# Kernel tuning notes

Hardware: AMD Instinct MI355X
Metric: run time of the kernel (lower is better)

## Reference

```python
import jax, jax.numpy as jnp
import numpy as np

B, H, W, DM = 4, 64, 64, 96
DS, DC, K = 16, 3, 4
DI = DM            # expand = 1.0
DTR = 6            # ceil(96/16)


def setup_inputs() -> dict:
    key = jax.random.key(0)
    ks = jax.random.split(key, 12)
    s = 0.02
    # dt bias init exactly as MS2D.dt_init: dt ~ exp(U*(log(max)-log(min))+log(min)); inv softplus
    dt = jnp.exp(jax.random.uniform(ks[5], (K, DI)) * (np.log(0.1) - np.log(0.001)) + np.log(0.001))
    dt = jnp.clip(dt, 1e-4, None)
    inv_dt = dt + jnp.log(-jnp.expm1(-dt))
    A_logs = jnp.log(jnp.broadcast_to(jnp.arange(1, DS + 1, dtype=jnp.float32), (K, DI, DS)))
    return {
        "x": jax.random.normal(ks[0], (B, H, W, DM), jnp.float32),
        "in_proj_w": jax.random.normal(ks[1], (2 * DI, DM), jnp.float32) * s,
        "conv_w": jax.random.normal(ks[2], (DI, 1, DC, DC), jnp.float32) * s,
        "conv_b": jnp.zeros((DI,), jnp.float32),
        "x_proj_weight": jax.random.normal(ks[3], (K, DTR + 2 * DS, DI), jnp.float32) * s,
        "dt_projs_weight": jax.random.uniform(ks[4], (K, DI, DTR), minval=-1.0, maxval=1.0) * (DTR ** -0.5),
        "dt_projs_bias": inv_dt,
        "A_logs": A_logs,
        "Ds": jnp.ones((K, DI), jnp.float32),
        "out_norm_w": jnp.ones((DI,), jnp.float32),
        "out_norm_b": jnp.zeros((DI,), jnp.float32),
        "out_proj_w": jax.random.normal(ks[6], (DM, DI), jnp.float32) * s,
    }


def _ms2d(x, in_proj_w, conv_w, conv_b, x_proj_weight, dt_projs_weight,
          dt_projs_bias, A_logs, Ds, out_norm_w, out_norm_b, out_proj_w):
    Bb, Hh, Ww, _ = x.shape
    L = Hh * Ww
    # in_proj -> (x, z) gating split
    xz = x @ in_proj_w.T                      # (B,H,W,2*DI)
    xc, z = jnp.split(xz, 2, axis=-1)
    xc = jnp.transpose(xc, (0, 3, 1, 2))      # (B,DI,H,W)
    xc = jax.lax.conv_general_dilated(
        xc, conv_w, (1, 1), 'SAME', feature_group_count=xc.shape[1],
        dimension_numbers=('NCHW', 'OIHW', 'NCHW')) + conv_b[None, :, None, None]
    xc = jax.nn.silu(xc)
    d = xc.shape[1]
    # 4-directional scan sequences: hw, wh, and their reverses
    x_hw = xc.reshape(Bb, d, L)
    x_wh = jnp.transpose(xc, (0, 1, 3, 2)).reshape(Bb, d, L)
    x2 = jnp.stack([x_hw, x_wh], axis=1)          # (B,2,d,L)
    xs = jnp.concatenate([x2, jnp.flip(x2, axis=-1)], axis=1)  # (B,4,d,L)
    x_dbl = jnp.einsum('bkdl,kcd->bkcl', xs, x_proj_weight)
    dtr = dt_projs_weight.shape[2]
    n = A_logs.shape[2]
    dts, Bs, Cs = jnp.split(x_dbl, [dtr, dtr + n], axis=2)     # (B,4,r,L),(B,4,N,L),(B,4,N,L)
    dts = jnp.einsum('bkrl,kdr->bkdl', dts, dt_projs_weight)
    delta = jax.nn.softplus(dts + dt_projs_bias[None, :, :, None])  # (B,4,d,L)
    A = -jnp.exp(A_logs)                                        # (4,d,N)
    # time-major for scan
    u_t = jnp.moveaxis(xs, -1, 0)       # (L,B,4,d)
    dl_t = jnp.moveaxis(delta, -1, 0)
    B_t = jnp.moveaxis(Bs, -1, 0)       # (L,B,4,N)
    C_t = jnp.moveaxis(Cs, -1, 0)

    def step(h, inp):                   # h: (B,4,d,N)
        u, dl, b, c = inp
        dA = jnp.exp(dl[..., None] * A)
        h = h * dA + (dl * u)[..., None] * b[:, :, None, :]
        y = jnp.einsum('bkdn,bkn->bkd', h, c)
        return h, y

    h0 = jnp.zeros((Bb, 4, d, n), xs.dtype)
    _, ys = jax.lax.scan(step, h0, (u_t, dl_t, B_t, C_t))
    ys = jnp.moveaxis(ys, 0, -1)        # (B,4,d,L)
    ys = ys + Ds[None, :, :, None] * xs  # skip D*u
    inv_y = jnp.flip(ys[:, 2:4], axis=-1)

    def wh2hw(t):  # undo the (W,H) raster order
        return jnp.transpose(t.reshape(Bb, d, Ww, Hh), (0, 1, 3, 2)).reshape(Bb, d, L)

    y = ys[:, 0] + inv_y[:, 0] + wh2hw(ys[:, 1]) + wh2hw(inv_y[:, 1])
    y = jnp.transpose(y, (0, 2, 1)).reshape(Bb, Hh, Ww, d)
    mu = y.mean(-1, keepdims=True)
    var = y.var(-1, keepdims=True)
    y = (y - mu) / jnp.sqrt(var + 1e-5) * out_norm_w + out_norm_b
    y = y * jax.nn.silu(z)
    return y @ out_proj_w.T


def reference(x, in_proj_w, conv_w, conv_b, x_proj_weight, dt_projs_weight,
              dt_projs_bias, A_logs, Ds, out_norm_w, out_norm_b, out_proj_w):
    return _ms2d(x, in_proj_w, conv_w, conv_b, x_proj_weight, dt_projs_weight,
                 dt_projs_bias, A_logs, Ds, out_norm_w, out_norm_b, out_proj_w)
```

## Files before the change

### kernel.cpp

```cpp
#include <hip/hip_runtime.h>
#include <math.h>


#define LQ 4096
#define NCH 128
#define LCH 32

__device__ __forceinline__ float sigmoid_f(float x){ return 1.0f/(1.0f + __expf(-x)); }
__device__ __forceinline__ float silu_f(float x){ return x * sigmoid_f(x); }
__device__ __forceinline__ float softplus_f(float x){ return (x > 20.0f) ? x : __logf(1.0f + __expf(x)); }

__device__ __forceinline__ int pos_of(int k, int i){
  switch(k & 3){
    case 0: return i;
    case 1: return ((i & 63) << 6) | (i >> 6);
    case 2: return LQ - 1 - i;
    default: { int j = LQ - 1 - i; return ((j & 63) << 6) | (j >> 6); }
  }
}

__device__ __forceinline__ void pow8(float r, int nh, float* e){
  e[0]=r;
  e[1]=r*r;
  e[2]=e[1]*r;
  e[3]=e[1]*e[1];
  e[4]=e[3]*r;
  e[5]=e[3]*e[1];
  e[6]=e[3]*e[2];
  e[7]=e[3]*e[3];
  float m = nh ? e[7] : 1.0f;
  #pragma unroll
  for (int j=0;j<8;j++) e[j] *= m;
}

__global__ __launch_bounds__(256) void k_inproj(const float* __restrict__ x,
                                                const float* __restrict__ wproj,
                                                float* __restrict__ xc,
                                                float* __restrict__ zb){
  __shared__ float a_s[64*97];
  __shared__ float w_s[96*97];
  const int t = threadIdx.x;
  const int row0 = (blockIdx.x >> 1) * 64;
  const int ch = blockIdx.x & 1;
  for (int e = t*4; e < 64*96; e += 1024){
    float4 v = *(const float4*)(x + (size_t)row0*96 + e);
    int r = e/96, c = e%96;
    float* p = a_s + r*97 + c;
    p[0]=v.x; p[1]=v.y; p[2]=v.z; p[3]=v.w;
  }
  for (int e = t*4; e < 96*96; e += 1024){
    float4 v = *(const float4*)(wproj + (size_t)ch*96*96 + e);
    int r = e/96, c = e%96;
    float* p = w_s + r*97 + c;
    p[0]=v.x; p[1]=v.y; p[2]=v.z; p[3]=v.w;
  }
  __syncthreads();
  const int tr = t >> 5, tc = t & 31;
  float acc[8][3];
  #pragma unroll
  for (int i=0;i<8;i++){
    #pragma unroll
    for (int j=0;j<3;j++) acc[i][j]=0.f;
  }
  for (int kk=0; kk<96; kk++){
    float a[8], b[3];
    #pragma unroll
    for (int i=0;i<8;i++) a[i] = a_s[(tr*8+i)*97+kk];
    #pragma unroll
    for (int j=0;j<3;j++) b[j] = w_s[(tc*3+j)*97+kk];
    #pragma unroll
    for (int i=0;i<8;i++){
      #pragma unroll
      for (int j=0;j<3;j++) acc[i][j] += a[i]*b[j];
    }
  }
  float* dst = ch ? zb : xc;
  #pragma unroll
  for (int i=0;i<8;i++){
    int row = row0 + tr*8 + i;
    #pragma unroll
    for (int j=0;j<3;j++) dst[(size_t)row*96 + tc*3 + j] = acc[i][j];
  }
}

__global__ __launch_bounds__(256) void k_conv(const float* __restrict__ xc,
                                              const float* __restrict__ cw,
                                              const float* __restrict__ cb,
                                              float* __restrict__ u){
  int e = blockIdx.x*256 + threadIdx.x;
  int d0 = (e % 24) * 4;
  int p = e / 24;
  int w = p & 63, h = (p >> 6) & 63, b = p >> 12;
  float cwv[4][9];
  #pragma unroll
  for (int q=0;q<4;q++){
    #pragma unroll
    for (int tp=0;tp<9;tp++) cwv[q][tp] = cw[(d0+q)*9+tp];
  }
  float4 acc = make_float4(cb[d0], cb[d0+1], cb[d0+2], cb[d0+3]);
  #pragma unroll
  for (int kh=0; kh<3; kh++){
    int hh = h + kh - 1;
    if (hh < 0 || hh > 63) continue;
    #pragma unroll
    for (int kw=0; kw<3; kw++){
      int ww = w + kw - 1;
      if (ww < 0 || ww > 63) continue;
      float4 v = *(const float4*)(xc + ((size_t)((b<<12) + (hh<<6) + ww))*96 + d0);
      int tp = kh*3+kw;
      acc.x += v.x*cwv[0][tp]; acc.y += v.y*cwv[1][tp];
      acc.z += v.z*cwv[2][tp]; acc.w += v.w*cwv[3][tp];
    }
  }
  float4 o = make_float4(silu_f(acc.x), silu_f(acc.y), silu_f(acc.z), silu_f(acc.w));
  *(float4*)(u + (size_t)p*96 + d0) = o;
}

__global__ __launch_bounds__(128) void k_proj(const float* __restrict__ u,
                                              const float* __restrict__ xpw,
                                              float* __restrict__ dts,
                                              float* __restrict__ Bsb,
                                              float* __restrict__ Csb){
  __shared__ float u_s[64*97];
  __shared__ float w_s[40*97];
  const int t = threadIdx.x;
  const int blk = blockIdx.x;
  const int pt = blk & 63, k = (blk >> 6) & 3, b = blk >> 8;
  const int p0 = pt * 64;
  for (int e = t*4; e < 64*96; e += 512){
    int pp = e/96, c = e%96;
    float4 v = *(const float4*)(u + ((size_t)((b<<12) + p0 + pp))*96 + c);
    float* p = u_s + pp*97 + c;
    p[0]=v.x; p[1]=v.y; p[2]=v.z; p[3]=v.w;
  }
  for (int e = t*4; e < 40*96; e += 512){
    int r = e/96, c = e%96;
    float4 v = (r < 38) ? *(const float4*)(xpw + (k*38+r)*96 + c)
                        : make_float4(0,0,0,0);
    float* p = w_s + r*97 + c;
    p[0]=v.x; p[1]=v.y; p[2]=v.z; p[3]=v.w;
  }
  __syncthreads();
  const int posg = t & 15, cg = t >> 4;
  float acc[4][5];
  #pragma unroll
  for (int i=0;i<4;i++){
    #pragma unroll
    for (int j=0;j<5;j++) acc[i][j]=0.f;
  }
  for (int dd=0; dd<96; dd++){
    float uu[4], wv[5];
    #pragma unroll
    for (int i=0;i<4;i++) uu[i] = u_s[(posg*4+i)*97+dd];
    #pragma unroll
    for (int j=0;j<5;j++) wv[j] = w_s[(cg*5+j)*97+dd];
    #pragma unroll
    for (int i=0;i<4;i++){
      #pragma unroll
      for (int j=0;j<5;j++) acc[i][j] += uu[i]*wv[j];
    }
  }
  #pragma unroll
  for (int i=0;i<4;i++){
    int p = p0 + posg*4 + i;
    int base = ((b*4+k)<<12) + p;
    #pragma unroll
    for (int j=0;j<5;j++){
      int c = cg*5 + j;
      float v = acc[i][j];
      if (c < 6)       dts[(size_t)base*6 + c] = v;
      else if (c < 22) Bsb[(size_t)base*16 + (c-6)] = v;
      else if (c < 38) Csb[(size_t)base*16 + (c-22)] = v;
    }
  }
}

__global__ __launch_bounds__(384) void k_scanA(const float* __restrict__ u,
                                               const float* __restrict__ dts,
                                               const float* __restrict__ Bsb,
                                               const float* __restrict__ dtw_g,
                                               const float* __restrict__ dtb_g,
                                               const float* __restrict__ Alogs,
                                               float* __restrict__ S,
                                               float* __restrict__ sumd){
  __shared__ float du_s[64*96];
  __shared__ float r_s[64*96];
  __shared__ float dt_s[64*8];
  __shared__ float B_s[64*16];
  __shared__ float sd_part[4*96];
  const int t = threadIdx.x;
  const int blk = blockIdx.x;
  const int bk = blk >> 6;
  const int k = bk & 3, b = bk >> 2;
  const int chunk0 = (blk & 63) << 1;
  for (int e = t*4; e < 64*96; e += 1536){
    int row = e/96, c = e%96;
    int p = pos_of(k, (chunk0 + (row>>5))*LCH + (row&31));
    float4 v = *(const float4*)(u + ((size_t)((b<<12)+p))*96 + c);
    float* dst = du_s + row*96 + c;
    dst[0]=v.x; dst[1]=v.y; dst[2]=v.z; dst[3]=v.w;
  }
  {
    int row = t/6, j = t - row*6;
    int p = pos_of(k, (chunk0 + (row>>5))*LCH + (row&31));
    dt_s[row*8+j] = dts[((size_t)((bk<<12)+p))*6 + j];
  }
  if (t < 256){
    int row = t>>2, q = t&3;
    int p = pos_of(k, (chunk0 + (row>>5))*LCH + (row&31));
    float4 v = *(const float4*)(Bsb + ((size_t)((bk<<12)+p))*16 + q*4);
    *(float4*)(B_s + row*16 + q*4) = v;
  }
  __syncthreads();
  {
    const int d = t % 96, g = t / 96;
    const int c2 = g >> 1, il0 = (g & 1) * 16;
    float dtwv[6];
    #pragma unroll
    for (int r=0;r<6;r++) dtwv[r] = dtw_g[(k*96+d)*6+r];
    const float bias = dtb_g[k*96+d];
    float sd = 0.f;
    #pragma unroll 4
    for (int il = il0; il < il0+16; il++){
      int row = c2*32 + il;
      const float* dr = dt_s + row*8;
      float accd = bias + dr[0]*dtwv[0] + dr[1]*dtwv[1] + dr[2]*dtwv[2]
                        + dr[3]*dtwv[3] + dr[4]*dtwv[4] + dr[5]*dtwv[5];
      float delta = softplus_f(accd);
      sd += delta;
      int idx = row*96 + d;
      du_s[idx] = delta * du_s[idx];
      r_s[idx] = __expf(-delta);
    }
    sd_part[g*96 + d] = sd;
  }
  __syncthreads();
  const int c2 = t / 192;
  const int lane = t & 63;
  const int wv3 = (t % 192) >> 6;
  const int nh = (lane >> 5) & 1;
  const int d = wv3*32 + (lane & 31);
  float An[8];
  bool fast = true;
  #pragma unroll
  for (int j=0;j<8;j++){
    int n = nh*8 + j;
    An[j] = -__expf(Alogs[(k*96+d)*16+n]);
    fast = fast && (fabsf(An[j] + (float)(n+1)) < 1e-3f*(float)(n+1));
  }
  int wfast = __all(fast ? 1 : 0);
  float h[8];
  #pragma unroll
  for (int n=0;n<8;n++) h[n]=0.f;
  const float* dup = du_s + c2*32*96 + d;
  const float* rp  = r_s  + c2*32*96 + d;
  const float* Bb  = B_s + c2*32*16 + nh*8;
  if (wfast){
    #pragma unroll 4
    for (int il=0; il<LCH; il++){
      float r = rp[il*96];
      float du = dup[il*96];
      const float4* Bp = (const float4*)(Bb + il*16);
      float4 b0 = Bp[0], b1 = Bp[1];
      float Bv[8] = {b0.x,b0.y,b0.z,b0.w, b1.x,b1.y,b1.z,b1.w};
      float e[8];
      pow8(r, nh, e);
      #pragma unroll
      for (int n=0;n<8;n++) h[n] = h[n]*e[n] + du*Bv[n];
    }
  } else {
    #pragma unroll 2
    for (int il=0; il<LCH; il++){
      float r = rp[il*96];
      float delta = -__logf(r);
      float du = dup[il*96];
      const float4* Bp = (const float4*)(Bb + il*16);
      float4 b0 = Bp[0], b1 = Bp[1];
      float Bv[8] = {b0.x,b0.y,b0.z,b0.w, b1.x,b1.y,b1.z,b1.w};
      float e[8];
      #pragma unroll
      for (int n=0;n<8;n++) e[n] = __expf(delta*An[n]);
      #pragma unroll
      for (int n=0;n<8;n++) h[n] = h[n]*e[n] + du*Bv[n];
    }
  }
  const int sb = (bk*NCH + chunk0 + c2)*96 + d;
  float4* Sp = (float4*)(S + (size_t)sb*16 + nh*8);
  Sp[0] = make_float4(h[0],h[1],h[2],h[3]);
  Sp[1] = make_float4(h[4],h[5],h[6],h[7]);
  if (nh == 0) sumd[sb] = sd_part[(c2*2)*96 + d] + sd_part[(c2*2+1)*96 + d];
}

__global__ __launch_bounds__(256) void k_scanB(const float* __restrict__ S,
                                               const float* __restrict__ sumd,
                                               const float* __restrict__ Alogs,
                                               float* __restrict__ hinit){
  const int t = blockIdx.x*256 + threadIdx.x;
  const int n = t & 15;
  const int d = (t >> 4) % 96;
  const int bk = t / 1536;
  const int k = bk & 3;
  const float An = -__expf(Alogs[(k*96+d)*16+n]);
  float h = 0.f;
  for (int c=0;c<NCH;c++){
    const int sb = (bk*NCH + c)*96 + d;
    hinit[(size_t)sb*16+n] = h;
    float P = __expf(An * sumd[sb]);
    h = h*P + S[(size_t)sb*16+n];
  }
}

__global__ __launch_bounds__(384) void k_scanC(const float* __restrict__ u,
                                               const float* __restrict__ dts,
                                               const float* __restrict__ Bsb,
                                               const float* __restrict__ Csb,
                                               const float* __restrict__ dtw_g,
                                               const float* __restrict__ dtb_g,
                                               const float* __restrict__ Alogs,
                                               const float* __restrict__ hinit,
                                               float* __restrict__ ys){
  __shared__ float du_s[64*96];
  __shared__ float r_s[64*96];
  __shared__ float dt_s[64*8];
  __shared__ float B_s[64*16];
  __shared__ float C_s[64*16];
  const int t = threadIdx.x;
  const int blk = blockIdx.x;
  const int bk = blk >> 6;
  const int k = bk & 3, b = bk >> 2;
  const int chunk0 = (blk & 63) << 1;
  for (int e = t*4; e < 64*96; e += 1536){
    int row = e/96, c = e%96;
    int p = pos_of(k, (chunk0 + (row>>5))*LCH + (row&31));
    float4 v = *(const float4*)(u + ((size_t)((b<<12)+p))*96 + c);
    float* dst = du_s + row*96 + c;
    dst[0]=v.x; dst[1]=v.y; dst[2]=v.z; dst[3]=v.w;
  }
  {
    int row = t/6, j = t - row*6;
    int p = pos_of(k, (chunk0 + (row>>5))*LCH + (row&31));
    dt_s[row*8+j] = dts[((size_t)((bk<<12)+p))*6 + j];
  }
  if (t < 256){
    int row = t>>2, q = t&3;
    int p = pos_of(k, (chunk0 + (row>>5))*LCH + (row&31));
    float4 v = *(const float4*)(Bsb + ((size_t)((bk<<12)+p))*16 + q*4);
    *(float4*)(B_s + row*16 + q*4) = v;
    float4 w = *(const float4*)(Csb + ((size_t)((bk<<12)+p))*16 + q*4);
    *(float4*)(C_s + row*16 + q*4) = w;
  }
  __syncthreads();
  {
    const int d = t % 96, g = t / 96;
    const int c2 = g >> 1, il0 = (g & 1) * 16;
    float dtwv[6];
    #pragma unroll
    for (int r=0;r<6;r++) dtwv[r] = dtw_g[(k*96+d)*6+r];
    const float bias = dtb_g[k*96+d];
    #pragma unroll 4
    for (int il = il0; il < il0+16; il++){
      int row = c2*32 + il;
      const float* dr = dt_s + row*8;
      float accd = bias + dr[0]*dtwv[0] + dr[1]*dtwv[1] + dr[2]*dtwv[2]
                        + dr[3]*dtwv[3] + dr[4]*dtwv[4] + dr[5]*dtwv[5];
      float delta = softplus_f(accd);
      int idx = row*96 + d;
      du_s[idx] = delta * du_s[idx];
      r_s[idx] = __expf(-delta);
    }
  }
  __syncthreads();
  const int c2 = t / 192;
  const int lane = t & 63;
  const int wv3 = (t % 192) >> 6;
  const int nh = (lane >> 5) & 1;
  const int d = wv3*32 + (lane & 31);
  float An[8];
  bool fast = true;
  #pragma unroll
  for (int j=0;j<8;j++){
    int n = nh*8 + j;
    An[j] = -__expf(Alogs[(k*96+d)*16+n]);
    fast = fast && (fabsf(An[j] + (float)(n+1)) < 1e-3f*(float)(n+1));
  }
  int wfast = __all(fast ? 1 : 0);
  const int chunk = chunk0 + c2;
  const int i0 = chunk*LCH;
  const int pb = pos_of(k, i0);
  const int pstep = pos_of(k, i0+1) - pb;
  float* yp = ys + ((size_t)((bk<<12)+pb))*96 + d;
  const long ystep = (long)pstep*96;
  float h[8];
  const int sb = (bk*NCH + chunk)*96 + d;
  const float4* Hp = (const float4*)(hinit + (size_t)sb*16 + nh*8);
  {
    float4 h0=Hp[0], h1=Hp[1];
    h[0]=h0.x;h[1]=h0.y;h[2]=h0.z;h[3]=h0.w;
    h[4]=h1.x;h[5]=h1.y;h[6]=h1.z;h[7]=h1.w;
  }
  const float* dup = du_s + c2*32*96 + d;
  const float* rp  = r_s  + c2*32*96 + d;
  const float* Bb  = B_s + c2*32*16 + nh*8;
  const float* Cb  = C_s + c2*32*16 + nh*8;
  if (wfast){
    #pragma unroll 4
    for (int il=0; il<LCH; il++){
      float r = rp[il*96];
      float du = dup[il*96];
      const float4* Bp = (const float4*)(Bb + il*16);
      const float4* Cp = (const float4*)(Cb + il*16);
      float4 b0 = Bp[0], b1 = Bp[1];
      float4 c0 = Cp[0], c1 = Cp[1];
      float Bv[8] = {b0.x,b0.y,b0.z,b0.w, b1.x,b1.y,b1.z,b1.w};
      float Cv[8] = {c0.x,c0.y,c0.z,c0.w, c1.x,c1.y,c1.z,c1.w};
      float e[8];
      pow8(r, nh, e);
      float y8 = 0.f;
      #pragma unroll
      for (int n=0;n<8;n++){
        h[n] = h[n]*e[n] + du*Bv[n];
        y8 += h[n]*Cv[n];
      }
      float y = y8 + __shfl_xor(y8, 32, 64);
      if (nh == 0) yp[il*ystep] = y;
    }
  } else {
    #pragma unroll 2
    for (int il=0; il<LCH; il++){
      float r = rp[il*96];
      float delta = -__logf(r);
      float du = dup[il*96];
      const float4* Bp = (const float4*)(Bb + il*16);
      const float4* Cp = (const float4*)(Cb + il*16);
      float4 b0 = Bp[0], b1 = Bp[1];
      float4 c0 = Cp[0], c1 = Cp[1];
      float Bv[8] = {b0.x,b0.y,b0.z,b0.w, b1.x,b1.y,b1.z,b1.w};
      float Cv[8] = {c0.x,c0.y,c0.z,c0.w, c1.x,c1.y,c1.z,c1.w};
      float e[8];
      #pragma unroll
      for (int n=0;n<8;n++) e[n] = __expf(delta*An[n]);
      float y8 = 0.f;
      #pragma unroll
      for (int n=0;n<8;n++){
        h[n] = h[n]*e[n] + du*Bv[n];
        y8 += h[n]*Cv[n];
      }
      float y = y8 + __shfl_xor(y8, 32, 64);
      if (nh == 0) yp[il*ystep] = y;
    }
  }
}

__global__ __launch_bounds__(256) void k_out(const float* __restrict__ ys,
                                             const float* __restrict__ ubuf,
                                             const float* __restrict__ Dsg,
                                             const float* __restrict__ zbuf,
                                             const float* __restrict__ nw,
                                             const float* __restrict__ nb,
                                             const float* __restrict__ wout,
                                             float* __restrict__ out){
  __shared__ float w_s[96*97];
  __shared__ float g_s[32*97];
  const int t = threadIdx.x;
  const int b = blockIdx.x >> 7;
  const int pt = blockIdx.x & 127;
  const int p0 = pt * 32;
  for (int e=t*4; e<96*96; e+=1024){
    float4 v = *(const float4*)(wout+e);
    int r=e/96, c=e%96;
    float* p = w_s + r*97 + c;
    p[0]=v.x; p[1]=v.y; p[2]=v.z; p[3]=v.w;
  }
  const int pos = t >> 3, lane8 = t & 7, d0 = lane8*12;
  const int p = p0 + pos;
  float yv[12];
  float s1=0.f, s2=0.f;
  #pragma unroll
  for (int i=0;i<12;i+=4){
    float4 a = make_float4(0,0,0,0);
    #pragma unroll
    for (int kk=0;kk<4;kk++){
      float4 v = *(const float4*)(ys + ((size_t)(((b*4+kk)<<12) + p))*96 + d0 + i);
      a.x+=v.x; a.y+=v.y; a.z+=v.z; a.w+=v.w;
    }
    float4 uv = *(const float4*)(ubuf + ((size_t)((b<<12)+p))*96 + d0 + i);
    #pragma unroll
    for (int q=0;q<4;q++){
      int dd = d0+i+q;
      float sD = Dsg[dd] + Dsg[96+dd] + Dsg[192+dd] + Dsg[288+dd];
      float uq = (q==0)?uv.x:(q==1)?uv.y:(q==2)?uv.z:uv.w;
      float* aq = (q==0)?&a.x:(q==1)?&a.y:(q==2)?&a.z:&a.w;
      *aq += sD * uq;
    }
    yv[i]=a.x; yv[i+1]=a.y; yv[i+2]=a.z; yv[i+3]=a.w;
    s1 += a.x+a.y+a.z+a.w;
    s2 += a.x*a.x + a.y*a.y + a.z*a.z + a.w*a.w;
  }
  #pragma unroll
  for (int m=1; m<8; m<<=1){
    s1 += __shfl_xor(s1, m, 64);
    s2 += __shfl_xor(s2, m, 64);
  }
  const float mu = s1 * (1.0f/96.0f);
  const float var = s2 * (1.0f/96.0f) - mu*mu;
  const float rstd = rsqrtf(var + 1e-5f);
  #pragma unroll
  for (int i=0;i<12;i+=4){
    float4 zv = *(const float4*)(zbuf + ((size_t)((b<<12)+p))*96 + d0 + i);
    float zz[4] = {zv.x,zv.y,zv.z,zv.w};
    #pragma unroll
    for (int q=0;q<4;q++){
      int d = d0+i+q;
      float yn = (yv[i+q]-mu)*rstd*nw[d] + nb[d];
      g_s[pos*97 + d] = yn * silu_f(zz[q]);
    }
  }
  __syncthreads();
  const int posg = t >> 5, mg = t & 31;
  float acc[4][3];
  #pragma unroll
  for (int i=0;i<4;i++){
    #pragma unroll
    for (int j=0;j<3;j++) acc[i][j]=0.f;
  }
  for (int dd=0; dd<96; dd++){
    float g4[4], w3[3];
    #pragma unroll
    for (int i=0;i<4;i++) g4[i] = g_s[(posg*4+i)*97+dd];
    #pragma unroll
    for (int j=0;j<3;j++) w3[j] = w_s[(mg*3+j)*97+dd];
    #pragma unroll
    for (int i=0;i<4;i++){
      #pragma unroll
      for (int j=0;j<3;j++) acc[i][j] += g4[i]*w3[j];
    }
  }
  #pragma unroll
  for (int i=0;i<4;i++){
    int prow = p0 + posg*4 + i;
    #pragma unroll
    for (int j=0;j<3;j++){
      out[((size_t)((b<<12)+prow))*96 + mg*3 + j] = acc[i][j];
    }
  }
}

extern "C" void kernel_launch(void* const* d_in, const int* in_sizes, int n_in,
                              void* d_out, int out_size, void* d_ws, size_t ws_size,
                              hipStream_t stream) {
  (void)in_sizes; (void)n_in; (void)out_size; (void)ws_size;
  const float* x   = (const float*)d_in[0];
  const float* ipw = (const float*)d_in[1];
  const float* cw  = (const float*)d_in[2];
  const float* cb  = (const float*)d_in[3];
  const float* xpw = (const float*)d_in[4];
  const float* dtw = (const float*)d_in[5];
  const float* dtb = (const float*)d_in[6];
  const float* alg = (const float*)d_in[7];
  const float* dsg = (const float*)d_in[8];
  const float* nw  = (const float*)d_in[9];
  const float* nb  = (const float*)d_in[10];
  const float* wo  = (const float*)d_in[11];
  float* out = (float*)d_out;

  float* w = (float*)d_ws;
  size_t off = 0;
  float* z_b    = w + off; off += 1572864;
  float* u_b    = w + off; off += 1572864;
  float* dts_b  = w + off; off += 393216;
  float* Bs_b   = w + off; off += 1048576;
  float* Cs_b   = w + off; off += 1048576;
  float* hin_b  = w + off; off += 3145728;
  float* ys_b   = w + off; off += 6291456;
  float* xc_b   = ys_b;
  float* S_b    = ys_b + 1572864;
  float* sumd_b = ys_b + 1572864 + 3145728;

  k_inproj<<<512, 256, 0, stream>>>(x, ipw, xc_b, z_b);
  k_conv  <<<1536, 256, 0, stream>>>(xc_b, cw, cb, u_b);
  k_proj  <<<1024, 128, 0, stream>>>(u_b, xpw, dts_b, Bs_b, Cs_b);
  k_scanA <<<1024, 384, 0, stream>>>(u_b, dts_b, Bs_b, dtw, dtb, alg, S_b, sumd_b);
  k_scanB <<<96, 256, 0, stream>>>(S_b, sumd_b, alg, hin_b);
  k_scanC <<<1024, 384, 0, stream>>>(u_b, dts_b, Bs_b, Cs_b, dtw, dtb, alg, hin_b, ys_b);
  k_out   <<<512, 256, 0, stream>>>(ys_b, u_b, dsg, z_b, nw, nb, wo, out);
}
```

Before: 241.1 us.

## Stream scan inputs from scan-ordered global buffers instead of staging in LDS

```diff
diff --git a/kernel.cpp b/kernel.cpp
--- a/kernel.cpp
+++ b/kernel.cpp
@@ -120,18 +120,22 @@
                                               const float* __restrict__ xpw,
                                               float* __restrict__ dts,
                                               float* __restrict__ Bsb,
-                                              float* __restrict__ Csb){
+                                              float* __restrict__ Csb,
+                                              float* __restrict__ us){
   __shared__ float u_s[64*97];
   __shared__ float w_s[40*97];
   const int t = threadIdx.x;
   const int blk = blockIdx.x;
   const int pt = blk & 63, k = (blk >> 6) & 3, b = blk >> 8;
-  const int p0 = pt * 64;
+  const int bk = b*4 + k;
+  const int i0 = pt * 64;
   for (int e = t*4; e < 64*96; e += 512){
-    int pp = e/96, c = e%96;
-    float4 v = *(const float4*)(u + ((size_t)((b<<12) + p0 + pp))*96 + c);
-    float* p = u_s + pp*97 + c;
-    p[0]=v.x; p[1]=v.y; p[2]=v.z; p[3]=v.w;
+    int row = e/96, c = e%96;
+    int p = pos_of(k, i0 + row);
+    float4 v = *(const float4*)(u + ((size_t)((b<<12) + p))*96 + c);
+    float* dst = u_s + row*97 + c;
+    dst[0]=v.x; dst[1]=v.y; dst[2]=v.z; dst[3]=v.w;
+    if (us) *(float4*)(us + ((size_t)((bk<<12) + i0 + row))*96 + c) = v;
   }
   for (int e = t*4; e < 40*96; e += 512){
     int r = e/96, c = e%96;
@@ -162,8 +166,8 @@
   }
   #pragma unroll
   for (int i=0;i<4;i++){
-    int p = p0 + posg*4 + i;
-    int base = ((b*4+k)<<12) + p;
+    int ii = i0 + posg*4 + i;
+    int base = (bk<<12) + ii;
     #pragma unroll
     for (int j=0;j<5;j++){
       int c = cg*5 + j;
@@ -176,6 +180,7 @@
 }
 
 __global__ __launch_bounds__(384) void k_scanA(const float* __restrict__ u,
+                                               const float* __restrict__ us,
                                                const float* __restrict__ dts,
                                                const float* __restrict__ Bsb,
                                                const float* __restrict__ dtw_g,
@@ -183,63 +188,17 @@
                                                const float* __restrict__ Alogs,
                                                float* __restrict__ S,
                                                float* __restrict__ sumd){
-  __shared__ float du_s[64*96];
-  __shared__ float r_s[64*96];
-  __shared__ float dt_s[64*8];
-  __shared__ float B_s[64*16];
-  __shared__ float sd_part[4*96];
   const int t = threadIdx.x;
-  const int blk = blockIdx.x;
-  const int bk = blk >> 6;
-  const int k = bk & 3, b = bk >> 2;
-  const int chunk0 = (blk & 63) << 1;
-  for (int e = t*4; e < 64*96; e += 1536){
-    int row = e/96, c = e%96;
-    int p = pos_of(k, (chunk0 + (row>>5))*LCH + (row&31));
-    float4 v = *(const float4*)(u + ((size_t)((b<<12)+p))*96 + c);
-    float* dst = du_s + row*96 + c;
-    dst[0]=v.x; dst[1]=v.y; dst[2]=v.z; dst[3]=v.w;
-  }
-  {
-    int row = t/6, j = t - row*6;
-    int p = pos_of(k, (chunk0 + (row>>5))*LCH + (row&31));
-    dt_s[row*8+j] = dts[((size_t)((bk<<12)+p))*6 + j];
-  }
-  if (t < 256){
-    int row = t>>2, q = t&3;
-    int p = pos_of(k, (chunk0 + (row>>5))*LCH + (row&31));
-    float4 v = *(const float4*)(Bsb + ((size_t)((bk<<12)+p))*16 + q*4);
-    *(float4*)(B_s + row*16 + q*4) = v;
-  }
-  __syncthreads();
-  {
-    const int d = t % 96, g = t / 96;
-    const int c2 = g >> 1, il0 = (g & 1) * 16;
-    float dtwv[6];
-    #pragma unroll
-    for (int r=0;r<6;r++) dtwv[r] = dtw_g[(k*96+d)*6+r];
-    const float bias = dtb_g[k*96+d];
-    float sd = 0.f;
-    #pragma unroll 4
-    for (int il = il0; il < il0+16; il++){
-      int row = c2*32 + il;
-      const float* dr = dt_s + row*8;
-      float accd = bias + dr[0]*dtwv[0] + dr[1]*dtwv[1] + dr[2]*dtwv[2]
-                        + dr[3]*dtwv[3] + dr[4]*dtwv[4] + dr[5]*dtwv[5];
-      float delta = softplus_f(accd);
-      sd += delta;
-      int idx = row*96 + d;
-      du_s[idx] = delta * du_s[idx];
-      r_s[idx] = __expf(-delta);
-    }
-    sd_part[g*96 + d] = sd;
-  }
-  __syncthreads();
   const int c2 = t / 192;
   const int lane = t & 63;
   const int wv3 = (t % 192) >> 6;
   const int nh = (lane >> 5) & 1;
   const int d = wv3*32 + (lane & 31);
+  const int blk = blockIdx.x;
+  const int bk = blk >> 6;
+  const int k = bk & 3, b = bk >> 2;
+  const int chunk = ((blk & 63) << 1) | c2;
+  const int ibase = chunk * LCH;
   float An[8];
   bool fast = true;
   #pragma unroll
@@ -249,32 +208,53 @@
     fast = fast && (fabsf(An[j] + (float)(n+1)) < 1e-3f*(float)(n+1));
   }
   int wfast = __all(fast ? 1 : 0);
+  float dtw[6];
+  #pragma unroll
+  for (int r=0;r<6;r++) dtw[r] = dtw_g[(k*96+d)*6+r];
+  const float bias = dtb_g[k*96+d];
+  const float* uptr; long ustep;
+  if (us){ uptr = us + ((size_t)((bk<<12)+ibase))*96 + d; ustep = 96; }
+  else {
+    int pb = pos_of(k, ibase);
+    int pstep = pos_of(k, ibase+1) - pb;
+    uptr = u + ((size_t)((b<<12)+pb))*96 + d; ustep = (long)pstep*96;
+  }
+  const float2* dtp = (const float2*)(dts + ((size_t)((bk<<12)+ibase))*6);
+  const float4* Bp = (const float4*)(Bsb + ((size_t)((bk<<12)+ibase))*16) + nh*2;
   float h[8];
   #pragma unroll
   for (int n=0;n<8;n++) h[n]=0.f;
-  const float* dup = du_s + c2*32*96 + d;
-  const float* rp  = r_s  + c2*32*96 + d;
-  const float* Bb  = B_s + c2*32*16 + nh*8;
+  float sdelta = 0.f;
   if (wfast){
     #pragma unroll 4
     for (int il=0; il<LCH; il++){
-      float r = rp[il*96];
-      float du = dup[il*96];
-      const float4* Bp = (const float4*)(Bb + il*16);
+      float uv = *uptr;
+      float2 q0 = dtp[0], q1 = dtp[1], q2 = dtp[2];
+      float accd = bias + dtw[0]*q0.x + dtw[1]*q0.y + dtw[2]*q1.x
+                        + dtw[3]*q1.y + dtw[4]*q2.x + dtw[5]*q2.y;
+      float t1 = __expf(accd);
+      float r = 1.0f / (1.0f + t1);
+      float delta = (accd > 20.f) ? accd : __logf(1.0f + t1);
+      sdelta += delta;
+      float du = delta * uv;
       float4 b0 = Bp[0], b1 = Bp[1];
       float Bv[8] = {b0.x,b0.y,b0.z,b0.w, b1.x,b1.y,b1.z,b1.w};
       float e[8];
       pow8(r, nh, e);
       #pragma unroll
       for (int n=0;n<8;n++) h[n] = h[n]*e[n] + du*Bv[n];
+      uptr += ustep; dtp += 3; Bp += 4;
     }
   } else {
     #pragma unroll 2
     for (int il=0; il<LCH; il++){
-      float r = rp[il*96];
-      float delta = -__logf(r);
-      float du = dup[il*96];
-      const float4* Bp = (const float4*)(Bb + il*16);
+      float uv = *uptr;
+      float2 q0 = dtp[0], q1 = dtp[1], q2 = dtp[2];
+      float accd = bias + dtw[0]*q0.x + dtw[1]*q0.y + dtw[2]*q1.x
+                        + dtw[3]*q1.y + dtw[4]*q2.x + dtw[5]*q2.y;
+      float delta = softplus_f(accd);
+      sdelta += delta;
+      float du = delta * uv;
       float4 b0 = Bp[0], b1 = Bp[1];
       float Bv[8] = {b0.x,b0.y,b0.z,b0.w, b1.x,b1.y,b1.z,b1.w};
       float e[8];
@@ -282,19 +262,20 @@
       for (int n=0;n<8;n++) e[n] = __expf(delta*An[n]);
       #pragma unroll
       for (int n=0;n<8;n++) h[n] = h[n]*e[n] + du*Bv[n];
-    }
-  }
-  const int sb = (bk*NCH + chunk0 + c2)*96 + d;
+      uptr += ustep; dtp += 3; Bp += 4;
+    }
+  }
+  const int sb = (bk*NCH + chunk)*96 + d;
   float4* Sp = (float4*)(S + (size_t)sb*16 + nh*8);
   Sp[0] = make_float4(h[0],h[1],h[2],h[3]);
   Sp[1] = make_float4(h[4],h[5],h[6],h[7]);
-  if (nh == 0) sumd[sb] = sd_part[(c2*2)*96 + d] + sd_part[(c2*2+1)*96 + d];
-}
-
-__global__ __launch_bounds__(256) void k_scanB(const float* __restrict__ S,
+  if (nh == 0) sumd[sb] = sdelta;
+}
+
+__global__ __launch_bounds__(256) void k_scanB(float* __restrict__ S,
                                                const float* __restrict__ sumd,
                                                const float* __restrict__ Alogs,
-                                               float* __restrict__ hinit){
+                                               float* ){
   const int t = blockIdx.x*256 + threadIdx.x;
   const int n = t & 15;
   const int d = (t >> 4) % 96;
@@ -304,77 +285,35 @@
   float h = 0.f;
   for (int c=0;c<NCH;c++){
     const int sb = (bk*NCH + c)*96 + d;
-    hinit[(size_t)sb*16+n] = h;
+    const size_t idx = (size_t)sb*16 + n;
+    float sOld = S[idx];
     float P = __expf(An * sumd[sb]);
-    h = h*P + S[(size_t)sb*16+n];
+    S[idx] = h;
+    h = h*P + sOld;
   }
 }
 
 __global__ __launch_bounds__(384) void k_scanC(const float* __restrict__ u,
+                                               const float* __restrict__ us,
                                                const float* __restrict__ dts,
                                                const float* __restrict__ Bsb,
                                                const float* __restrict__ Csb,
                                                const float* __restrict__ dtw_g,
                                                const float* __restrict__ dtb_g,
                                                const float* __restrict__ Alogs,
-                                               const float* __restrict__ hinit,
+                                               const float* __restrict__ h0buf,
                                                float* __restrict__ ys){
-  __shared__ float du_s[64*96];
-  __shared__ float r_s[64*96];
-  __shared__ float dt_s[64*8];
-  __shared__ float B_s[64*16];
-  __shared__ float C_s[64*16];
   const int t = threadIdx.x;
-  const int blk = blockIdx.x;
-  const int bk = blk >> 6;
-  const int k = bk & 3, b = bk >> 2;
-  const int chunk0 = (blk & 63) << 1;
-  for (int e = t*4; e < 64*96; e += 1536){
-    int row = e/96, c = e%96;
-    int p = pos_of(k, (chunk0 + (row>>5))*LCH + (row&31));
-    float4 v = *(const float4*)(u + ((size_t)((b<<12)+p))*96 + c);
-    float* dst = du_s + row*96 + c;
-    dst[0]=v.x; dst[1]=v.y; dst[2]=v.z; dst[3]=v.w;
-  }
-  {
-    int row = t/6, j = t - row*6;
-    int p = pos_of(k, (chunk0 + (row>>5))*LCH + (row&31));
-    dt_s[row*8+j] = dts[((size_t)((bk<<12)+p))*6 + j];
-  }
-  if (t < 256){
-    int row = t>>2, q = t&3;
-    int p = pos_of(k, (chunk0 + (row>>5))*LCH + (row&31));
-    float4 v = *(const float4*)(Bsb + ((size_t)((bk<<12)+p))*16 + q*4);
-    *(float4*)(B_s + row*16 + q*4) = v;
-    float4 w = *(const float4*)(Csb + ((size_t)((bk<<12)+p))*16 + q*4);
-    *(float4*)(C_s + row*16 + q*4) = w;
-  }
-  __syncthreads();
-  {
-    const int d = t % 96, g = t / 96;
-    const int c2 = g >> 1, il0 = (g & 1) * 16;
-    float dtwv[6];
-    #pragma unroll
-    for (int r=0;r<6;r++) dtwv[r] = dtw_g[(k*96+d)*6+r];
-    const float bias = dtb_g[k*96+d];
-    #pragma unroll 4
-    for (int il = il0; il < il0+16; il++){
-      int row = c2*32 + il;
-      const float* dr = dt_s + row*8;
-      float accd = bias + dr[0]*dtwv[0] + dr[1]*dtwv[1] + dr[2]*dtwv[2]
-                        + dr[3]*dtwv[3] + dr[4]*dtwv[4] + dr[5]*dtwv[5];
-      float delta = softplus_f(accd);
-      int idx = row*96 + d;
-      du_s[idx] = delta * du_s[idx];
-      r_s[idx] = __expf(-delta);
-    }
-  }
-  __syncthreads();
   const int c2 = t / 192;
   const int lane = t & 63;
   const int wv3 = (t % 192) >> 6;
   const int nh = (lane >> 5) & 1;
   const int d = wv3*32 + (lane & 31);
+  const int blk = blockIdx.x;
+  const int bk = blk >> 6;
+  const int k = bk & 3, b = bk >> 2;
+  const int chunk = ((blk & 63) << 1) | c2;
+  const int ibase = chunk * LCH;
   float An[8];
   bool fast = true;
   #pragma unroll
@@ -384,31 +323,39 @@
     fast = fast && (fabsf(An[j] + (float)(n+1)) < 1e-3f*(float)(n+1));
   }
   int wfast = __all(fast ? 1 : 0);
-  const int chunk = chunk0 + c2;
-  const int i0 = chunk*LCH;
-  const int pb = pos_of(k, i0);
-  const int pstep = pos_of(k, i0+1) - pb;
+  float dtw[6];
+  #pragma unroll
+  for (int r=0;r<6;r++) dtw[r] = dtw_g[(k*96+d)*6+r];
+  const float bias = dtb_g[k*96+d];
+  const int pb = pos_of(k, ibase);
+  const int pstep = pos_of(k, ibase+1) - pb;
+  const float* uptr; long ustep;
+  if (us){ uptr = us + ((size_t)((bk<<12)+ibase))*96 + d; ustep = 96; }
+  else   { uptr = u + ((size_t)((b<<12)+pb))*96 + d; ustep = (long)pstep*96; }
+  const float2* dtp = (const float2*)(dts + ((size_t)((bk<<12)+ibase))*6);
+  const float4* Bp = (const float4*)(Bsb + ((size_t)((bk<<12)+ibase))*16) + nh*2;
+  const float4* Cp = (const float4*)(Csb + ((size_t)((bk<<12)+ibase))*16) + nh*2;
   float* yp = ys + ((size_t)((bk<<12)+pb))*96 + d;
   const long ystep = (long)pstep*96;
   float h[8];
   const int sb = (bk*NCH + chunk)*96 + d;
-  const float4* Hp = (const float4*)(hinit + (size_t)sb*16 + nh*8);
+  const float4* Hp = (const float4*)(h0buf + (size_t)sb*16 + nh*8);
   {
     float4 h0=Hp[0], h1=Hp[1];
     h[0]=h0.x;h[1]=h0.y;h[2]=h0.z;h[3]=h0.w;
     h[4]=h1.x;h[5]=h1.y;h[6]=h1.z;h[7]=h1.w;
   }
-  const float* dup = du_s + c2*32*96 + d;
-  const float* rp  = r_s  + c2*32*96 + d;
-  const float* Bb  = B_s + c2*32*16 + nh*8;
-  const float* Cb  = C_s + c2*32*16 + nh*8;
   if (wfast){
     #pragma unroll 4
     for (int il=0; il<LCH; il++){
-      float r = rp[il*96];
-      float du = dup[il*96];
-      const float4* Bp = (const float4*)(Bb + il*16);
-      const float4* Cp = (const float4*)(Cb + il*16);
+      float uv = *uptr;
+      float2 q0 = dtp[0], q1 = dtp[1], q2 = dtp[2];
+      float accd = bias + dtw[0]*q0.x + dtw[1]*q0.y + dtw[2]*q1.x
+                        + dtw[3]*q1.y + dtw[4]*q2.x + dtw[5]*q2.y;
+      float t1 = __expf(accd);
+      float r = 1.0f / (1.0f + t1);
+      float delta = (accd > 20.f) ? accd : __logf(1.0f + t1);
+      float du = delta * uv;
       float4 b0 = Bp[0], b1 = Bp[1];
       float4 c0 = Cp[0], c1 = Cp[1];
       float Bv[8] = {b0.x,b0.y,b0.z,b0.w, b1.x,b1.y,b1.z,b1.w};
@@ -423,15 +370,17 @@
       }
       float y = y8 + __shfl_xor(y8, 32, 64);
       if (nh == 0) yp[il*ystep] = y;
+      uptr += ustep; dtp += 3; Bp += 4; Cp += 4;
     }
   } else {
     #pragma unroll 2
     for (int il=0; il<LCH; il++){
-      float r = rp[il*96];
-      float delta = -__logf(r);
-      float du = dup[il*96];
-      const float4* Bp = (const float4*)(Bb + il*16);
-      const float4* Cp = (const float4*)(Cb + il*16);
+      float uv = *uptr;
+      float2 q0 = dtp[0], q1 = dtp[1], q2 = dtp[2];
+      float accd = bias + dtw[0]*q0.x + dtw[1]*q0.y + dtw[2]*q1.x
+                        + dtw[3]*q1.y + dtw[4]*q2.x + dtw[5]*q2.y;
+      float delta = softplus_f(accd);
+      float du = delta * uv;
       float4 b0 = Bp[0], b1 = Bp[1];
       float4 c0 = Cp[0], c1 = Cp[1];
       float Bv[8] = {b0.x,b0.y,b0.z,b0.w, b1.x,b1.y,b1.z,b1.w};
@@ -447,6 +396,7 @@
       }
       float y = y8 + __shfl_xor(y8, 32, 64);
       if (nh == 0) yp[il*ystep] = y;
+      uptr += ustep; dtp += 3; Bp += 4; Cp += 4;
     }
   }
 }
@@ -548,7 +498,7 @@
 extern "C" void kernel_launch(void* const* d_in, const int* in_sizes, int n_in,
                               void* d_out, int out_size, void* d_ws, size_t ws_size,
                               hipStream_t stream) {
-  (void)in_sizes; (void)n_in; (void)out_size; (void)ws_size;
+  (void)in_sizes; (void)n_in; (void)out_size;
   const float* x   = (const float*)d_in[0];
   const float* ipw = (const float*)d_in[1];
   const float* cw  = (const float*)d_in[2];
@@ -570,17 +520,18 @@
   float* dts_b  = w + off; off += 393216;
   float* Bs_b   = w + off; off += 1048576;
   float* Cs_b   = w + off; off += 1048576;
-  float* hin_b  = w + off; off += 3145728;
+  float* Sh_b   = w + off; off += 3145728;
+  float* sumd_b = w + off; off += 98304;
   float* ys_b   = w + off; off += 6291456;
   float* xc_b   = ys_b;
-  float* S_b    = ys_b + 1572864;
-  float* sumd_b = ys_b + 1572864 + 3145728;
+  size_t need_us = (off + 6291456) * sizeof(float);
+  float* us_b = (ws_size >= need_us) ? (w + off) : nullptr;
 
   k_inproj<<<512, 256, 0, stream>>>(x, ipw, xc_b, z_b);
   k_conv  <<<1536, 256, 0, stream>>>(xc_b, cw, cb, u_b);
-  k_proj  <<<1024, 128, 0, stream>>>(u_b, xpw, dts_b, Bs_b, Cs_b);
-  k_scanA <<<1024, 384, 0, stream>>>(u_b, dts_b, Bs_b, dtw, dtb, alg, S_b, sumd_b);
-  k_scanB <<<96, 256, 0, stream>>>(S_b, sumd_b, alg, hin_b);
-  k_scanC <<<1024, 384, 0, stream>>>(u_b, dts_b, Bs_b, Cs_b, dtw, dtb, alg, hin_b, ys_b);
+  k_proj  <<<1024, 128, 0, stream>>>(u_b, xpw, dts_b, Bs_b, Cs_b, us_b);
+  k_scanA <<<1024, 384, 0, stream>>>(u_b, us_b, dts_b, Bs_b, dtw, dtb, alg, Sh_b, sumd_b);
+  k_scanB <<<96, 256, 0, stream>>>(Sh_b, sumd_b, alg, nullptr);
+  k_scanC <<<1024, 384, 0, stream>>>(u_b, us_b, dts_b, Bs_b, Cs_b, dtw, dtb, alg, Sh_b, ys_b);
   k_out   <<<512, 256, 0, stream>>>(ys_b, u_b, dsg, z_b, nw, nb, wo, out);
 }
```

Result: no change. 241.4 us (+0.1%).
